# Performance work log

Measured on AMD Instinct MI355X. Metric: run time of the kernel, lower is better.

## Reference

```python
import jax, jax.numpy as jnp
import numpy as np

B, N, F = 32, 64, 128          # batch, num_nodes, n_in_node
K, H, M, NH = 4, 256, 256, 256 # edge_types, msg_hid, msg_out, n_hid
E = N * (N - 1)                # fully-connected directed edges = 4032


def setup_inputs() -> dict:
    key = jax.random.key(0)
    ks = jax.random.split(key, 12)
    inputs = jax.random.normal(ks[0], (B, N, F), dtype=jnp.float32)
    # soft edge-type assignment per edge (rows sum to 1, as in NRI)
    rel_type = jax.nn.softmax(jax.random.normal(ks[1], (B, E, K), dtype=jnp.float32), axis=-1)
    # one-hot receiver/sender matrices for all i != j pairs
    idx = np.array([(i, j) for i in range(N) for j in range(N) if i != j], dtype=np.int64)
    eye = np.eye(N, dtype=np.float32)
    rel_rec = jnp.asarray(eye[idx[:, 0]])   # [E, N]
    rel_send = jnp.asarray(eye[idx[:, 1]])  # [E, N]
    # per-edge-type message MLP weights (stacked over K): y = x @ W + b
    W1 = jax.random.normal(ks[2], (K, 2 * F, H), dtype=jnp.float32) / np.sqrt(2 * F)
    b1 = jnp.zeros((K, H), dtype=jnp.float32)
    W2 = jax.random.normal(ks[3], (K, H, M), dtype=jnp.float32) / np.sqrt(H)
    b2 = jnp.zeros((K, M), dtype=jnp.float32)
    # output MLP
    Wo1 = jax.random.normal(ks[4], (F + M, NH), dtype=jnp.float32) / np.sqrt(F + M)
    bo1 = jnp.zeros((NH,), dtype=jnp.float32)
    Wo2 = jax.random.normal(ks[5], (NH, NH), dtype=jnp.float32) / np.sqrt(NH)
    bo2 = jnp.zeros((NH,), dtype=jnp.float32)
    Wo3 = jax.random.normal(ks[6], (NH, F), dtype=jnp.float32) / np.sqrt(NH)
    bo3 = jnp.zeros((F,), dtype=jnp.float32)
    return {"inputs": inputs, "rel_type": rel_type, "rel_rec": rel_rec, "rel_send": rel_send,
            "W1": W1, "b1": b1, "W2": W2, "b2": b2,
            "Wo1": Wo1, "bo1": bo1, "Wo2": Wo2, "bo2": bo2, "Wo3": Wo3, "bo3": bo3}


def reference(inputs, rel_type, rel_rec, rel_send, W1, b1, W2, b2, Wo1, bo1, Wo2, bo2, Wo3, bo3):
    # gather node states to edges via one-hot matmul (as in the source)
    receivers = jnp.einsum('en,bnf->bef', rel_rec, inputs)   # [B,E,F]
    senders = jnp.einsum('en,bnf->bef', rel_send, inputs)    # [B,E,F]
    pre_msg = jnp.concatenate([receivers, senders], axis=-1)  # [B,E,2F]
    # per-edge-type 2-layer ReLU MLP, batched over the K edge types
    h = jax.nn.relu(jnp.einsum('bef,kfh->bkeh', pre_msg, W1) + b1[:, None, :])  # [B,K,E,H]
    msg = jax.nn.relu(jnp.einsum('bkeh,khm->bkem', h, W2) + b2[:, None, :])     # [B,K,E,M]
    # mask by soft edge type and accumulate over types (dropout p=0 -> identity)
    all_msgs = jnp.einsum('bkem,bek->bem', msg, rel_type)     # [B,E,M]
    # scatter-aggregate messages to receiver nodes via one-hot matmul
    agg_msgs = jnp.einsum('en,bem->bnm', rel_rec, all_msgs)   # [B,N,M]
    aug = jnp.concatenate([inputs, agg_msgs], axis=-1)        # [B,N,F+M]
    p = jax.nn.relu(aug @ Wo1 + bo1)
    p = jax.nn.relu(p @ Wo2 + bo2)
    p = p @ Wo3 + bo3
    return inputs + p
```

## Files before the change

kernel.cpp:

```cpp
#include <hip/hip_runtime.h>


#define B_ 32
#define N_ 64
#define F_ 128
#define K_ 4
#define E_ 4032

#define WS_W2T 0u
#define WS_R   524288u
#define WS_S   4718592u
#define WS_AGG 8912896u

typedef unsigned short u16;
typedef u16    u16x4  __attribute__((ext_vector_type(4)));
typedef u16    u16x8  __attribute__((ext_vector_type(8)));
typedef __bf16 bf16x8 __attribute__((ext_vector_type(8)));
typedef float  f32x4  __attribute__((ext_vector_type(4)));
typedef float  f32x16 __attribute__((ext_vector_type(16)));

__device__ __forceinline__ u16 f2bf(float f) {
    unsigned u; __builtin_memcpy(&u, &f, 4);
    return (u16)((u + 0x7FFFu + ((u >> 16) & 1u)) >> 16);
}
__device__ __forceinline__ float bf2f(u16 u) {
    unsigned v = ((unsigned)u) << 16;
    float f; __builtin_memcpy(&f, &v, 4); return f;
}
__device__ __forceinline__ void gl_lds16(const u16* g, u16* l) {
    __builtin_amdgcn_global_load_lds(
        (const __attribute__((address_space(1))) void*)g,
        (__attribute__((address_space(3))) void*)l, 16, 0, 0);
}

#define LBAR() do { \
    asm volatile("s_waitcnt lgkmcnt(0)" ::: "memory"); \
    __builtin_amdgcn_s_barrier(); \
    __builtin_amdgcn_sched_barrier(0); \
} while (0)

__global__ __launch_bounds__(256) void prep_rs_kernel(
    const float* __restrict__ W2, const float* __restrict__ x,
    const float* __restrict__ W1, const float* __restrict__ b1,
    u16* __restrict__ W2t, u16* __restrict__ R, u16* __restrict__ S)
{
    __shared__ u16 ldsA[64 * 136];
    __shared__ u16 ldsW[32 * 136];
    const int tid = threadIdx.x;

    if (blockIdx.x < 1024) {
        unsigned gid = blockIdx.x * 256u + tid;
        unsigned chunk = gid >> 13, r = gid & 8191u;
        unsigned g = r >> 11, n = (r >> 3) & 255u, e = r & 7u;
        unsigned k = chunk >> 3, kc = chunk & 7u, ks2 = g >> 1, lhh = g & 1u;
        unsigned kk = kc * 32u + ks2 * 16u + lhh * 8u + e;
        W2t[gid] = f2bf(W2[(k * 256u + kk) * 256u + n]);
        return;
    }

    const int lane = tid & 63, w = tid >> 6;
    const int quad = lane >> 4, mloc = lane & 15;
    const int bx = blockIdx.x - 1024;
    const int k = bx >> 6, half = (bx >> 5) & 1, b = bx & 31;

    for (int idx = tid; idx < 2048; idx += 256) {
        int row = idx >> 5, c4 = idx & 31;
        f32x4 v = *(const f32x4*)&x[(b * 64 + row) * 128 + c4 * 4];
        u16x4 o;
#pragma unroll
        for (int e = 0; e < 4; ++e) o[e] = f2bf(v[e]);
        *(u16x4*)&ldsA[row * 136 + c4 * 4] = o;
    }
    __syncthreads();

    bf16x8 aF[4];
#pragma unroll
    for (int ks = 0; ks < 4; ++ks)
        aF[ks] = *(const bf16x8*)&ldsA[(w * 16 + mloc) * 136 + quad * 8 + ks * 32];

    u16* dst = half ? S : R;
    for (int c = 0; c < 8; ++c) {
        __syncthreads();
        for (int idx = tid; idx < 4096; idx += 256) {
            int n = idx & 31, f = idx >> 5;
            ldsW[n * 136 + f] = f2bf(W1[(k * 256 + half * 128 + f) * 256 + c * 32 + n]);
        }
        __syncthreads();
#pragma unroll
        for (int nt = 0; nt < 2; ++nt) {
            f32x4 acc = (f32x4){0.f, 0.f, 0.f, 0.f};
            const int boff = (nt * 16 + mloc) * 136 + quad * 8;
#pragma unroll
            for (int ks = 0; ks < 4; ++ks)
                acc = __builtin_amdgcn_mfma_f32_16x16x32_bf16(
                    aF[ks], *(const bf16x8*)&ldsW[boff + ks * 32], acc, 0, 0, 0);
            const int n = c * 32 + nt * 16 + mloc;
            const float bias = half ? 0.f : b1[k * 256 + n];
#pragma unroll
            for (int r = 0; r < 4; ++r) {
                int row = w * 16 + quad * 4 + r;
                dst[(size_t)(k * 2048 + b * 64 + row) * 256 + n] = f2bf(acc[r] + bias);
            }
        }
    }
}

__global__ __launch_bounds__(256, 2) void edge7_kernel(
    const u16* __restrict__ R, const u16* __restrict__ S,
    const float* __restrict__ rel, const u16* __restrict__ W2t,
    const float* __restrict__ b2, u16* __restrict__ aggb)
{
    __shared__ u16   WtS[2][8192];
    __shared__ u16   HS[2][4][128][8];
    __shared__ float Rf[2][4][256];
    __shared__ float rtS[2][4][64];

    const int tid  = threadIdx.x;
    const int lane = tid & 63;
    const int w    = tid >> 6;
    const int l31  = lane & 31;
    const int lh   = lane >> 5;
    const int bid  = ((blockIdx.x & 7) << 7) | (blockIdx.x >> 3);
    const int b    = bid >> 5;
    const int i0   = (bid & 31) * 2;
    const int brow = tid >> 2;
    const int bc   = tid & 3;

    {
        const u16* src = W2t + w * 2048;
        u16* dst = &WtS[0][w * 2048];
#pragma unroll
        for (int it2 = 0; it2 < 4; ++it2)
            gl_lds16(src + it2 * 512 + lane * 8, dst + it2 * 512);
    }
    for (int t = tid; t < 512; t += 256) {
        int recv = t >> 8, rem = t & 255, k = rem >> 6, j = rem & 63;
        int i = i0 + recv;
        float v = 0.f;
        if (j != i) {
            int jj = j - (j > i);
            v = rel[((size_t)(b * E_) + i * 63 + jj) * 4 + k];
        }
        rtS[recv][k][j] = v;
    }
    {
        int recv = tid >> 7, k = (tid >> 5) & 3, e8 = tid & 31;
        u16x8 t8 = *(const u16x8*)&R[((size_t)(k * 2048 + b * 64 + i0 + recv)) * 256 + e8 * 8];
#pragma unroll
        for (int e = 0; e < 8; ++e) Rf[recv][k][e8 * 8 + e] = bf2f(t8[e]);
    }
    u16x8 sv = *(const u16x8*)&S[((size_t)(b * 64 + brow)) * 256 + bc * 8];
    __syncthreads();

    {
#pragma unroll
        for (int recv = 0; recv < 2; ++recv) {
            const float* rp = &Rf[recv][0][bc * 8];
            f32x4 r0 = *(const f32x4*)rp, r1 = *(const f32x4*)(rp + 4);
            bf16x8 o;
#pragma unroll
            for (int e = 0; e < 4; ++e) {
                o[e]     = (__bf16)fmaxf(r0[e] + bf2f(sv[e]),     0.f);
                o[4 + e] = (__bf16)fmaxf(r1[e] + bf2f(sv[4 + e]), 0.f);
            }
            *(bf16x8*)&HS[0][bc][recv * 64 + brow][0] = o;
        }
    }
    __syncthreads();

    float amsg[2][2] = {{0.f, 0.f}, {0.f, 0.f}};
    f32x16 acc[4][2];

    for (int it = 0; it < 32; ++it) {
        const int kT = it >> 3, kcT = it & 7;
        if (kcT == 0) {
#pragma unroll
            for (int mt = 0; mt < 4; ++mt)
#pragma unroll
                for (int nt = 0; nt < 2; ++nt) acc[mt][nt] = (f32x16)(0.f);
        }
        u16x8 svN;
        if (it < 31) {
            const u16* src = W2t + (size_t)(it + 1) * 8192 + w * 2048;
            u16* dst = &WtS[(it + 1) & 1][w * 2048];
#pragma unroll
            for (int it2 = 0; it2 < 4; ++it2)
                gl_lds16(src + it2 * 512 + lane * 8, dst + it2 * 512);
            const int kT2 = (it + 1) >> 3, kc2 = (it + 1) & 7;
            svN = *(const u16x8*)&S[((size_t)(kT2 * 2048 + b * 64 + brow)) * 256 + kc2 * 32 + bc * 8];
        }
        const u16* buf = WtS[it & 1];
        const u16(*hs)[128][8] = HS[it & 1];
#pragma unroll
        for (int ks2 = 0; ks2 < 2; ++ks2) {
            bf16x8 A[4], Bv[2];
#pragma unroll
            for (int mt = 0; mt < 4; ++mt)
                A[mt] = *(const bf16x8*)&hs[ks2 * 2 + lh][mt * 32 + l31][0];
#pragma unroll
            for (int nt = 0; nt < 2; ++nt)
                Bv[nt] = *(const bf16x8*)&buf[(ks2 * 2 + lh) * 2048 + (w * 64 + nt * 32 + l31) * 8];
#pragma unroll
            for (int mt = 0; mt < 4; ++mt)
#pragma unroll
                for (int nt = 0; nt < 2; ++nt)
                    acc[mt][nt] = __builtin_amdgcn_mfma_f32_32x32x16_bf16(A[mt], Bv[nt], acc[mt][nt], 0, 0, 0);
        }
        if (it < 31) {
            const int kT2 = (it + 1) >> 3, kc2 = (it + 1) & 7;
            const int db = (it + 1) & 1;
#pragma unroll
            for (int recv = 0; recv < 2; ++recv) {
                const float* rp = &Rf[recv][kT2][kc2 * 32 + bc * 8];
                f32x4 r0 = *(const f32x4*)rp, r1 = *(const f32x4*)(rp + 4);
                bf16x8 o;
#pragma unroll
                for (int e = 0; e < 4; ++e) {
                    o[e]     = (__bf16)fmaxf(r0[e] + bf2f(svN[e]),     0.f);
                    o[4 + e] = (__bf16)fmaxf(r1[e] + bf2f(svN[4 + e]), 0.f);
                }
                *(bf16x8*)&HS[db][bc][recv * 64 + brow][0] = o;
            }
        }
        if (kcT == 7) {
#pragma unroll
            for (int nt = 0; nt < 2; ++nt) {
                const float bias = b2[kT * 256 + w * 64 + nt * 32 + l31];
#pragma unroll
                for (int mt = 0; mt < 4; ++mt) {
                    const int recv = mt >> 1;
                    float s = 0.f;
#pragma unroll
                    for (int rq = 0; rq < 4; ++rq) {
                        f32x4 rt4 = *(const f32x4*)&rtS[recv][kT][(mt & 1) * 32 + rq * 8 + 4 * lh];
#pragma unroll
                        for (int e = 0; e < 4; ++e) {
                            float v = acc[mt][nt][rq * 4 + e] + bias;
                            v = v > 0.f ? v : 0.f;
                            s += rt4[e] * v;
                        }
                    }
                    amsg[recv][nt] += s;
                }
            }
        }
        __syncthreads();
    }

#pragma unroll
    for (int recv = 0; recv < 2; ++recv)
#pragma unroll
        for (int nt = 0; nt < 2; ++nt) {
            float s = amsg[recv][nt] + __shfl_xor(amsg[recv][nt], 32);
            if (lh == 0)
                aggb[(size_t)(b * 64 + i0 + recv) * 256 + w * 64 + nt * 32 + l31] = f2bf(s);
        }
}

__global__ __launch_bounds__(256) void outmlp3_kernel(
    const float* __restrict__ x, const u16* __restrict__ aggb,
    const float* __restrict__ Wo1, const float* __restrict__ bo1,
    const float* __restrict__ Wo2, const float* __restrict__ bo2,
    const float* __restrict__ Wo3, const float* __restrict__ bo3,
    float* __restrict__ out)
{
    __shared__ u16 wch[4][256][8];
    __shared__ u16 p1S[32 * 264];
    __shared__ u16 p2S[32 * 264];
    const int tid = threadIdx.x, lane = tid & 63, w = tid >> 6;
    const int quad = lane >> 4, mloc = lane & 15;
    const int row0 = blockIdx.x * 32;

    {
        f32x4 acc[2][4];
#pragma unroll
        for (int mt = 0; mt < 2; ++mt)
#pragma unroll
            for (int nt = 0; nt < 4; ++nt) acc[mt][nt] = (f32x4){0.f, 0.f, 0.f, 0.f};
        float wr[32];
#pragma unroll
        for (int g = 0; g < 4; ++g)
#pragma unroll
            for (int e = 0; e < 8; ++e) wr[g * 8 + e] = Wo1[(g * 8 + e) * 256 + tid];
        for (int kk = 0; kk < 12; ++kk) {
            bf16x8 aF[2];
#pragma unroll
            for (int mt = 0; mt < 2; ++mt) {
                const int row = row0 + mt * 16 + mloc;
                if (kk < 4) {
                    u16x8 t;
#pragma unroll
                    for (int e = 0; e < 8; ++e) t[e] = f2bf(x[row * 128 + kk * 32 + quad * 8 + e]);
                    __builtin_memcpy(&aF[mt], &t, 16);
                } else {
                    aF[mt] = *(const bf16x8*)&aggb[(size_t)row * 256 + (kk - 4) * 32 + quad * 8];
                }
            }
#pragma unroll
            for (int g = 0; g < 4; ++g) {
                u16x8 o;
#pragma unroll
                for (int e = 0; e < 8; ++e) o[e] = f2bf(wr[g * 8 + e]);
                *(u16x8*)&wch[g][tid][0] = o;
            }
            if (kk + 1 < 12) {
#pragma unroll
                for (int g = 0; g < 4; ++g)
#pragma unroll
                    for (int e = 0; e < 8; ++e) wr[g * 8 + e] = Wo1[((kk + 1) * 32 + g * 8 + e) * 256 + tid];
            }
            LBAR();
#pragma unroll
            for (int nt = 0; nt < 4; ++nt) {
                bf16x8 bF = *(const bf16x8*)&wch[quad][w * 64 + nt * 16 + mloc][0];
#pragma unroll
                for (int mt = 0; mt < 2; ++mt)
                    acc[mt][nt] = __builtin_amdgcn_mfma_f32_16x16x32_bf16(aF[mt], bF, acc[mt][nt], 0, 0, 0);
            }
            LBAR();
        }
#pragma unroll
        for (int nt = 0; nt < 4; ++nt) {
            const int n = w * 64 + nt * 16 + mloc;
            const float bias = bo1[n];
#pragma unroll
            for (int mt = 0; mt < 2; ++mt)
#pragma unroll
                for (int r = 0; r < 4; ++r) {
                    float v = acc[mt][nt][r] + bias;
                    p1S[(mt * 16 + quad * 4 + r) * 264 + n] = f2bf(v > 0.f ? v : 0.f);
                }
        }
    }
    LBAR();
    {
        f32x4 acc[2][4];
#pragma unroll
        for (int mt = 0; mt < 2; ++mt)
#pragma unroll
            for (int nt = 0; nt < 4; ++nt) acc[mt][nt] = (f32x4){0.f, 0.f, 0.f, 0.f};
        float wr[32];
#pragma unroll
        for (int g = 0; g < 4; ++g)
#pragma unroll
            for (int e = 0; e < 8; ++e) wr[g * 8 + e] = Wo2[(g * 8 + e) * 256 + tid];
        for (int kk = 0; kk < 8; ++kk) {
            bf16x8 aF[2];
#pragma unroll
            for (int mt = 0; mt < 2; ++mt)
                aF[mt] = *(const bf16x8*)&p1S[(mt * 16 + mloc) * 264 + kk * 32 + quad * 8];
#pragma unroll
            for (int g = 0; g < 4; ++g) {
                u16x8 o;
#pragma unroll
                for (int e = 0; e < 8; ++e) o[e] = f2bf(wr[g * 8 + e]);
                *(u16x8*)&wch[g][tid][0] = o;
            }
            if (kk + 1 < 8) {
#pragma unroll
                for (int g = 0; g < 4; ++g)
#pragma unroll
                    for (int e = 0; e < 8; ++e) wr[g * 8 + e] = Wo2[((kk + 1) * 32 + g * 8 + e) * 256 + tid];
            }
            LBAR();
#pragma unroll
            for (int nt = 0; nt < 4; ++nt) {
                bf16x8 bF = *(const bf16x8*)&wch[quad][w * 64 + nt * 16 + mloc][0];
#pragma unroll
                for (int mt = 0; mt < 2; ++mt)
                    acc[mt][nt] = __builtin_amdgcn_mfma_f32_16x16x32_bf16(aF[mt], bF, acc[mt][nt], 0, 0, 0);
            }
            LBAR();
        }
#pragma unroll
        for (int nt = 0; nt < 4; ++nt) {
            const int n = w * 64 + nt * 16 + mloc;
            const float bias = bo2[n];
#pragma unroll
            for (int mt = 0; mt < 2; ++mt)
#pragma unroll
                for (int r = 0; r < 4; ++r) {
                    float v = acc[mt][nt][r] + bias;
                    p2S[(mt * 16 + quad * 4 + r) * 264 + n] = f2bf(v > 0.f ? v : 0.f);
                }
        }
    }
    LBAR();
    {
        f32x4 acc[2][2];
#pragma unroll
        for (int mt = 0; mt < 2; ++mt)
#pragma unroll
            for (int nt = 0; nt < 2; ++nt) acc[mt][nt] = (f32x4){0.f, 0.f, 0.f, 0.f};
        const int sn = tid & 127, sh = tid >> 7;
        float wr[16];
#pragma unroll
        for (int g2 = 0; g2 < 2; ++g2)
#pragma unroll
            for (int e = 0; e < 8; ++e) wr[g2 * 8 + e] = Wo3[((sh * 2 + g2) * 8 + e) * 128 + sn];
        for (int kk = 0; kk < 8; ++kk) {
            bf16x8 aF[2];
#pragma unroll
            for (int mt = 0; mt < 2; ++mt)
                aF[mt] = *(const bf16x8*)&p2S[(mt * 16 + mloc) * 264 + kk * 32 + quad * 8];
#pragma unroll
            for (int g2 = 0; g2 < 2; ++g2) {
                const int g = sh * 2 + g2;
                u16x8 o;
#pragma unroll
                for (int e = 0; e < 8; ++e) o[e] = f2bf(wr[g2 * 8 + e]);
                *(u16x8*)&wch[g][sn][0] = o;
            }
            if (kk + 1 < 8) {
#pragma unroll
                for (int g2 = 0; g2 < 2; ++g2)
#pragma unroll
                    for (int e = 0; e < 8; ++e)
                        wr[g2 * 8 + e] = Wo3[((kk + 1) * 32 + (sh * 2 + g2) * 8 + e) * 128 + sn];
            }
            LBAR();
#pragma unroll
            for (int nt = 0; nt < 2; ++nt) {
                bf16x8 bF = *(const bf16x8*)&wch[quad][w * 32 + nt * 16 + mloc][0];
#pragma unroll
                for (int mt = 0; mt < 2; ++mt)
                    acc[mt][nt] = __builtin_amdgcn_mfma_f32_16x16x32_bf16(aF[mt], bF, acc[mt][nt], 0, 0, 0);
            }
            LBAR();
        }
#pragma unroll
        for (int nt = 0; nt < 2; ++nt) {
            const int n = w * 32 + nt * 16 + mloc;
            const float bias = bo3[n];
#pragma unroll
            for (int mt = 0; mt < 2; ++mt)
#pragma unroll
                for (int r = 0; r < 4; ++r) {
                    const int grow = row0 + mt * 16 + quad * 4 + r;
                    out[grow * 128 + n] = x[grow * 128 + n] + acc[mt][nt][r] + bias;
                }
        }
    }
}

extern "C" void kernel_launch(void* const* d_in, const int* in_sizes, int n_in,
                              void* d_out, int out_size, void* d_ws, size_t ws_size,
                              hipStream_t stream) {
    const float* x   = (const float*)d_in[0];
    const float* rel = (const float*)d_in[1];
    const float* W1  = (const float*)d_in[4];
    const float* b1  = (const float*)d_in[5];
    const float* W2  = (const float*)d_in[6];
    const float* b2  = (const float*)d_in[7];
    const float* Wo1 = (const float*)d_in[8];
    const float* bo1 = (const float*)d_in[9];
    const float* Wo2 = (const float*)d_in[10];
    const float* bo2 = (const float*)d_in[11];
    const float* Wo3 = (const float*)d_in[12];
    const float* bo3 = (const float*)d_in[13];
    float* out = (float*)d_out;

    char* ws = (char*)d_ws;
    u16* W2t  = (u16*)(ws + WS_W2T);
    u16* R    = (u16*)(ws + WS_R);
    u16* S    = (u16*)(ws + WS_S);
    u16* aggb = (u16*)(ws + WS_AGG);

    prep_rs_kernel<<<1280, 256, 0, stream>>>(W2, x, W1, b1, W2t, R, S);
    edge7_kernel<<<1024, 256, 0, stream>>>(R, S, rel, W2t, b2, aggb);
    outmlp3_kernel<<<64, 256, 0, stream>>>(x, aggb, Wo1, bo1, Wo2, bo2, Wo3, bo3, out);
}
```

Baseline: 207.3 us.

## Process one receiver per block and retile sender precompute for contiguous loads

The edge kernel now handles one receiver node per block instead of two, doubling the grid to 2048 blocks. It halves the per-block MFMA tile and LDS use so the launch bound can rise to three blocks per CU. The prep kernel now writes the sender projection in a chunked layout, so each per-iteration load of 32 columns is contiguous. The cost is that every W2 tile is streamed from global/L2 twice as often, since each W2 chunk is reused across only 64 edges instead of 128.

```diff
diff --git a/kernel.cpp b/kernel.cpp
--- a/kernel.cpp
+++ b/kernel.cpp
@@ -99,32 +99,35 @@
 #pragma unroll
             for (int r = 0; r < 4; ++r) {
                 int row = w * 16 + quad * 4 + r;
-                dst[(size_t)(k * 2048 + b * 64 + row) * 256 + n] = f2bf(acc[r] + bias);
-            }
-        }
-    }
-}
-
-__global__ __launch_bounds__(256, 2) void edge7_kernel(
-    const u16* __restrict__ R, const u16* __restrict__ S,
+                if (half) {
+                    dst[((size_t)((k * 8 + c) * 2048 + b * 64 + row)) * 32 + nt * 16 + mloc]
+                        = f2bf(acc[r] + bias);
+                } else {
+                    dst[((size_t)(k * 2048 + b * 64 + row)) * 256 + n] = f2bf(acc[r] + bias);
+                }
+            }
+        }
+    }
+}
+
+__global__ __launch_bounds__(256, 3) void edge9_kernel(
+    const u16* __restrict__ R, const u16* __restrict__ S2,
     const float* __restrict__ rel, const u16* __restrict__ W2t,
     const float* __restrict__ b2, u16* __restrict__ aggb)
 {
     __shared__ u16   WtS[2][8192];
-    __shared__ u16   HS[2][4][128][8];
-    __shared__ float Rf[2][4][256];
-    __shared__ float rtS[2][4][64];
+    __shared__ u16   HS[2][4][64][8];
+    __shared__ float Rf[4][256];
+    __shared__ float rtS[4][64];
 
     const int tid  = threadIdx.x;
     const int lane = tid & 63;
     const int w    = tid >> 6;
     const int l31  = lane & 31;
     const int lh   = lane >> 5;
-    const int bid  = ((blockIdx.x & 7) << 7) | (blockIdx.x >> 3);
-    const int b    = bid >> 5;
-    const int i0   = (bid & 31) * 2;
-    const int brow = tid >> 2;
-    const int bc   = tid & 3;
+    const int bid  = ((blockIdx.x & 7) << 8) | (blockIdx.x >> 3);
+    const int b    = bid >> 6;
+    const int i    = bid & 63;
 
     {
         const u16* src = W2t + w * 2048;
@@ -133,106 +136,89 @@
         for (int it2 = 0; it2 < 4; ++it2)
             gl_lds16(src + it2 * 512 + lane * 8, dst + it2 * 512);
     }
-    for (int t = tid; t < 512; t += 256) {
-        int recv = t >> 8, rem = t & 255, k = rem >> 6, j = rem & 63;
-        int i = i0 + recv;
+    {
+        const int k = tid >> 6, j = tid & 63;
         float v = 0.f;
-        if (j != i) {
-            int jj = j - (j > i);
-            v = rel[((size_t)(b * E_) + i * 63 + jj) * 4 + k];
-        }
-        rtS[recv][k][j] = v;
-    }
-    {
-        int recv = tid >> 7, k = (tid >> 5) & 3, e8 = tid & 31;
-        u16x8 t8 = *(const u16x8*)&R[((size_t)(k * 2048 + b * 64 + i0 + recv)) * 256 + e8 * 8];
-#pragma unroll
-        for (int e = 0; e < 8; ++e) Rf[recv][k][e8 * 8 + e] = bf2f(t8[e]);
-    }
-    u16x8 sv = *(const u16x8*)&S[((size_t)(b * 64 + brow)) * 256 + bc * 8];
+        if (j != i) v = rel[((size_t)(b * E_) + i * 63 + (j - (j > i))) * 4 + k];
+        rtS[k][j] = v;
+    }
+    {
+        const int k = tid >> 6, e4 = tid & 63;
+        u16x4 t4 = *(const u16x4*)&R[((size_t)(k * 2048 + b * 64 + i)) * 256 + e4 * 4];
+#pragma unroll
+        for (int e = 0; e < 4; ++e) Rf[k][e4 * 4 + e] = bf2f(t4[e]);
+    }
+    u16x8 sv = *(const u16x8*)&S2[((size_t)(b * 64 + lane)) * 32 + w * 8];
     __syncthreads();
 
     {
-#pragma unroll
-        for (int recv = 0; recv < 2; ++recv) {
-            const float* rp = &Rf[recv][0][bc * 8];
-            f32x4 r0 = *(const f32x4*)rp, r1 = *(const f32x4*)(rp + 4);
-            bf16x8 o;
-#pragma unroll
-            for (int e = 0; e < 4; ++e) {
-                o[e]     = (__bf16)fmaxf(r0[e] + bf2f(sv[e]),     0.f);
-                o[4 + e] = (__bf16)fmaxf(r1[e] + bf2f(sv[4 + e]), 0.f);
-            }
-            *(bf16x8*)&HS[0][bc][recv * 64 + brow][0] = o;
-        }
+        const float* rp = &Rf[0][w * 8];
+        f32x4 r0 = *(const f32x4*)rp, r1 = *(const f32x4*)(rp + 4);
+        bf16x8 o;
+#pragma unroll
+        for (int e = 0; e < 4; ++e) {
+            o[e]     = (__bf16)fmaxf(r0[e] + bf2f(sv[e]),     0.f);
+            o[4 + e] = (__bf16)fmaxf(r1[e] + bf2f(sv[4 + e]), 0.f);
+        }
+        *(bf16x8*)&HS[0][w][lane][0] = o;
     }
     __syncthreads();
 
-    float amsg[2][2] = {{0.f, 0.f}, {0.f, 0.f}};
-    f32x16 acc[4][2];
+    float amsg[2] = {0.f, 0.f};
+    f32x16 acc[2][2];
 
     for (int it = 0; it < 32; ++it) {
         const int kT = it >> 3, kcT = it & 7;
         if (kcT == 0) {
 #pragma unroll
-            for (int mt = 0; mt < 4; ++mt)
+            for (int mt = 0; mt < 2; ++mt)
 #pragma unroll
                 for (int nt = 0; nt < 2; ++nt) acc[mt][nt] = (f32x16)(0.f);
         }
         u16x8 svN;
         if (it < 31) {
+            svN = *(const u16x8*)&S2[((size_t)((it + 1) * 2048 + b * 64 + lane)) * 32 + w * 8];
             const u16* src = W2t + (size_t)(it + 1) * 8192 + w * 2048;
             u16* dst = &WtS[(it + 1) & 1][w * 2048];
 #pragma unroll
             for (int it2 = 0; it2 < 4; ++it2)
                 gl_lds16(src + it2 * 512 + lane * 8, dst + it2 * 512);
-            const int kT2 = (it + 1) >> 3, kc2 = (it + 1) & 7;
-            svN = *(const u16x8*)&S[((size_t)(kT2 * 2048 + b * 64 + brow)) * 256 + kc2 * 32 + bc * 8];
         }
         const u16* buf = WtS[it & 1];
-        const u16(*hs)[128][8] = HS[it & 1];
+        const u16(*hs)[64][8] = HS[it & 1];
 #pragma unroll
         for (int ks2 = 0; ks2 < 2; ++ks2) {
-            bf16x8 A[4], Bv[2];
-#pragma unroll
-            for (int mt = 0; mt < 4; ++mt)
-                A[mt] = *(const bf16x8*)&hs[ks2 * 2 + lh][mt * 32 + l31][0];
-#pragma unroll
-            for (int nt = 0; nt < 2; ++nt)
-                Bv[nt] = *(const bf16x8*)&buf[(ks2 * 2 + lh) * 2048 + (w * 64 + nt * 32 + l31) * 8];
-#pragma unroll
-            for (int mt = 0; mt < 4; ++mt)
-#pragma unroll
-                for (int nt = 0; nt < 2; ++nt)
-                    acc[mt][nt] = __builtin_amdgcn_mfma_f32_32x32x16_bf16(A[mt], Bv[nt], acc[mt][nt], 0, 0, 0);
+            bf16x8 A0 = *(const bf16x8*)&hs[ks2 * 2 + lh][l31][0];
+            bf16x8 A1 = *(const bf16x8*)&hs[ks2 * 2 + lh][32 + l31][0];
+            bf16x8 B0 = *(const bf16x8*)&buf[(ks2 * 2 + lh) * 2048 + (w * 64 + l31) * 8];
+            bf16x8 B1 = *(const bf16x8*)&buf[(ks2 * 2 + lh) * 2048 + (w * 64 + 32 + l31) * 8];
+            acc[0][0] = __builtin_amdgcn_mfma_f32_32x32x16_bf16(A0, B0, acc[0][0], 0, 0, 0);
+            acc[0][1] = __builtin_amdgcn_mfma_f32_32x32x16_bf16(A0, B1, acc[0][1], 0, 0, 0);
+            acc[1][0] = __builtin_amdgcn_mfma_f32_32x32x16_bf16(A1, B0, acc[1][0], 0, 0, 0);
+            acc[1][1] = __builtin_amdgcn_mfma_f32_32x32x16_bf16(A1, B1, acc[1][1], 0, 0, 0);
         }
         if (it < 31) {
             const int kT2 = (it + 1) >> 3, kc2 = (it + 1) & 7;
-            const int db = (it + 1) & 1;
-#pragma unroll
-            for (int recv = 0; recv < 2; ++recv) {
-                const float* rp = &Rf[recv][kT2][kc2 * 32 + bc * 8];
-                f32x4 r0 = *(const f32x4*)rp, r1 = *(const f32x4*)(rp + 4);
-                bf16x8 o;
-#pragma unroll
-                for (int e = 0; e < 4; ++e) {
-                    o[e]     = (__bf16)fmaxf(r0[e] + bf2f(svN[e]),     0.f);
-                    o[4 + e] = (__bf16)fmaxf(r1[e] + bf2f(svN[4 + e]), 0.f);
-                }
-                *(bf16x8*)&HS[db][bc][recv * 64 + brow][0] = o;
-            }
+            const float* rp = &Rf[kT2][kc2 * 32 + w * 8];
+            f32x4 r0 = *(const f32x4*)rp, r1 = *(const f32x4*)(rp + 4);
+            bf16x8 o;
+#pragma unroll
+            for (int e = 0; e < 4; ++e) {
+                o[e]     = (__bf16)fmaxf(r0[e] + bf2f(svN[e]),     0.f);
+                o[4 + e] = (__bf16)fmaxf(r1[e] + bf2f(svN[4 + e]), 0.f);
+            }
+            *(bf16x8*)&HS[(it + 1) & 1][w][lane][0] = o;
         }
         if (kcT == 7) {
 #pragma unroll
             for (int nt = 0; nt < 2; ++nt) {
                 const float bias = b2[kT * 256 + w * 64 + nt * 32 + l31];
 #pragma unroll
-                for (int mt = 0; mt < 4; ++mt) {
-                    const int recv = mt >> 1;
+                for (int mt = 0; mt < 2; ++mt) {
                     float s = 0.f;
 #pragma unroll
                     for (int rq = 0; rq < 4; ++rq) {
-                        f32x4 rt4 = *(const f32x4*)&rtS[recv][kT][(mt & 1) * 32 + rq * 8 + 4 * lh];
+                        f32x4 rt4 = *(const f32x4*)&rtS[kT][mt * 32 + rq * 8 + 4 * lh];
 #pragma unroll
                         for (int e = 0; e < 4; ++e) {
                             float v = acc[mt][nt][rq * 4 + e] + bias;
@@ -240,7 +226,7 @@
                             s += rt4[e] * v;
                         }
                     }
-                    amsg[recv][nt] += s;
+                    amsg[nt] += s;
                 }
             }
         }
@@ -248,13 +234,11 @@
     }
 
 #pragma unroll
-    for (int recv = 0; recv < 2; ++recv)
-#pragma unroll
-        for (int nt = 0; nt < 2; ++nt) {
-            float s = amsg[recv][nt] + __shfl_xor(amsg[recv][nt], 32);
-            if (lh == 0)
-                aggb[(size_t)(b * 64 + i0 + recv) * 256 + w * 64 + nt * 32 + l31] = f2bf(s);
-        }
+    for (int nt = 0; nt < 2; ++nt) {
+        float s = amsg[nt] + __shfl_xor(amsg[nt], 32);
+        if (lh == 0)
+            aggb[(size_t)(b * 64 + i) * 256 + w * 64 + nt * 32 + l31] = f2bf(s);
+    }
 }
 
 __global__ __launch_bounds__(256) void outmlp3_kernel(
@@ -463,10 +447,10 @@
     char* ws = (char*)d_ws;
     u16* W2t  = (u16*)(ws + WS_W2T);
     u16* R    = (u16*)(ws + WS_R);
-    u16* S    = (u16*)(ws + WS_S);
+    u16* S2   = (u16*)(ws + WS_S);
     u16* aggb = (u16*)(ws + WS_AGG);
 
-    prep_rs_kernel<<<1280, 256, 0, stream>>>(W2, x, W1, b1, W2t, R, S);
-    edge7_kernel<<<1024, 256, 0, stream>>>(R, S, rel, W2t, b2, aggb);
+    prep_rs_kernel<<<1280, 256, 0, stream>>>(W2, x, W1, b1, W2t, R, S2);
+    edge9_kernel<<<2048, 256, 0, stream>>>(R, S2, rel, W2t, b2, aggb);
     outmlp3_kernel<<<64, 256, 0, stream>>>(x, aggb, Wo1, bo1, Wo2, bo2, Wo3, bo3, out);
 }
```

New measurement: 224.6 us. 8.3% more time.
